# Kernel optimization log

Measured on AMD Instinct MI355X. Metric: run time of the kernel, lower is better.

The kernel has to match this reference:

```python
import jax, jax.numpy as jnp
import numpy as np

DEPTH = 6
N_LEAF = 2 ** DEPTH          # 64
GATE_COUNT = N_LEAF - 1      # 63
B = 1024
GATING_FEATURES = 512
IN_FEATURES = 512
OUT_FEATURES = 512


def setup_inputs() -> dict:
    key = jax.random.key(0)
    k1, k2, k3, k4 = jax.random.split(key, 4)
    x_gating = jax.random.normal(k1, (B, GATING_FEATURES), dtype=jnp.float32)
    x_leaf = jax.random.normal(k2, (B, IN_FEATURES), dtype=jnp.float32)
    # kaiming-normal-ish init scales
    gw = jax.random.normal(k3, (GATING_FEATURES, GATE_COUNT), dtype=jnp.float32) * (1.0 / np.sqrt(GATING_FEATURES))
    gb = jnp.zeros((GATE_COUNT,), dtype=jnp.float32)
    pw = jax.random.normal(k4, (OUT_FEATURES, IN_FEATURES, N_LEAF), dtype=jnp.float32) * (1.0 / np.sqrt(IN_FEATURES))
    pb = jnp.zeros((OUT_FEATURES, N_LEAF), dtype=jnp.float32)
    return {"x_gating": x_gating, "x_leaf": x_leaf, "gw": gw, "gb": gb, "pw": pw, "pb": pb}


def _leaf_probs(x_gating, gw, gb):
    # gatings: (B, gate_count), internal nodes in breadth-first order
    gatings = jax.nn.sigmoid(x_gating @ gw + gb)
    b = gatings.shape[0]
    dens = jnp.ones((b, 1), dtype=gatings.dtype)  # root density
    start = 0
    for d in range(DEPTH):
        n_par = 2 ** d
        g = gatings[:, start:start + n_par]          # (B, n_par)
        # left child (even it+1) gets g, right child gets 1-g, interleaved
        dens = jnp.stack([dens * g, dens * (1.0 - g)], axis=-1).reshape(b, 2 * n_par)
        start += n_par
    return dens  # (B, n_leaf) = leaf densities (last n_leaf node densities)


def reference(x_gating, x_leaf, gw, gb, pw, pb):
    leaf_probs = _leaf_probs(x_gating, gw, gb)              # (B, L)
    # gated projection applied to x_leaf, summed over leaves:
    # equals ((pw @ leaf_probs.T).permute(2,0,1) @ x_leaf[...,None])[...,0]
    result = jnp.einsum('oil,bl,bi->bo', pw, leaf_probs, x_leaf)
    result = result + leaf_probs @ pb.T                     # gated bias (B, O)
    return result
```

## Files before the change

kernel.cpp:

```cpp
#include <hip/hip_runtime.h>
#include <stdint.h>

#define B_SZ   1024
#define GF     512
#define GC     63
#define NLEAF  64
#define IN_F   512
#define OUT_F  512

typedef float f32x4 __attribute__((ext_vector_type(4)));
typedef __fp16 h16x2 __attribute__((ext_vector_type(2)));
typedef __fp16 h16x8 __attribute__((ext_vector_type(8)));
typedef _Float16 f16x2 __attribute__((ext_vector_type(2)));

union HF8 { f16x2 h2[4]; h16x8 v; uint4 u; };

__device__ inline f16x2 pkrtz(float a, float b) {
  union { h16x2 r; f16x2 f; } u;
  u.r = __builtin_amdgcn_cvt_pkrtz(a, b);
  return u.f;
}

__global__ __launch_bounds__(512, 2) void k_leafprobs(
    const float* __restrict__ xg, const float* __restrict__ gw,
    const float* __restrict__ gb, float* __restrict__ p_ws)
{
  __shared__ float xsr[GF];
  __shared__ float part[512];
  __shared__ float gates[GC + 1];
  const int b = blockIdx.x;
  const int t = threadIdx.x;

  xsr[t] = xg[(size_t)b * GF + t];
  __syncthreads();

  const int ks = t >> 6, g = t & 63;
  float acc = 0.f;
  if (g < GC) {
    const float* gp = gw + (size_t)(ks * 64) * GC + g;
    const float* xp = &xsr[ks * 64];
#pragma unroll 8
    for (int k = 0; k < 64; ++k) acc += xp[k] * gp[(size_t)k * GC];
  }
  part[t] = acc;
  __syncthreads();

  if (t < GC) {
    float s = gb[t];
#pragma unroll
    for (int r = 0; r < 8; ++r) s += part[r * 64 + t];
    gates[t] = 1.f / (1.f + expf(-s));
  }
  __syncthreads();

  if (t < NLEAF) {
    float v = 1.f;
    int idx = 0, start = 0;
#pragma unroll
    for (int d = 0; d < 6; ++d) {
      int bit = (t >> (5 - d)) & 1;
      float gg = gates[start + idx];
      v *= bit ? (1.f - gg) : gg;
      idx = 2 * idx + bit;
      start += (1 << d);
    }
    p_ws[(size_t)b * NLEAF + t] = v;
  }
}

#define SK 16
#define KI 32

template <bool ATOMIC>
__global__ __launch_bounds__(256, 2) void k_fused(
    const float* __restrict__ x_leaf,
    const float* __restrict__ p_ws,
    const float* __restrict__ pw,
    float* __restrict__ dst)
{
  __shared__ __align__(16) float         xs[KI][256];
  __shared__ __align__(16) unsigned char bs8[2 * 16384];

  const int tid  = threadIdx.x;
  const int lane = tid & 63;
  const int wid  = tid >> 6;
  const int quad = lane >> 4;
  const int l15  = lane & 15;
  const int l7   = l15 & 7;

  const int bid = blockIdx.x;
  const int nt  = bid & 7;
  const int mt  = (bid >> 3) & 3;
  const int kc  = bid >> 5;

  const int row_m0 = mt * 256;
  const int o0     = nt * 64;
  const int i0     = kc * KI;
  const int wm     = wid * 64;

  {
    const float* src = x_leaf + (size_t)(row_m0 + tid) * IN_F + i0;
#pragma unroll
    for (int q = 0; q < 8; ++q) {
      float4 v = *(const float4*)(src + q * 4);
      xs[q * 4 + 0][tid] = v.x;
      xs[q * 4 + 1][tid] = v.y;
      xs[q * 4 + 2][tid] = v.z;
      xs[q * 4 + 3][tid] = v.w;
    }
  }

  HF8 prh[4][2];
#pragma unroll
  for (int mi = 0; mi < 4; ++mi) {
    const int row = row_m0 + wm + mi * 16 + l15;
#pragma unroll
    for (int ks = 0; ks < 2; ++ks) {
      const f32x4* src = (const f32x4*)(p_ws + (size_t)row * NLEAF + ks * 32 + quad * 8);
      f32x4 lo = src[0], hi = src[1];
      prh[mi][ks].h2[0] = pkrtz(lo[0], lo[1]);
      prh[mi][ks].h2[1] = pkrtz(lo[2], lo[3]);
      prh[mi][ks].h2[2] = pkrtz(hi[0], hi[1]);
      prh[mi][ks].h2[3] = pkrtz(hi[2], hi[3]);
    }
  }

  const int br  = tid >> 2;
  const int seg = tid & 3;
  const float* bsrc0 = pw + ((size_t)(o0 + br) * IN_F + i0) * NLEAF + seg * 16;

  const int wsw   = (br & 7) << 4;
  const int woff0 = br * 128 + ((seg * 32) ^ wsw);
  const int woff1 = br * 128 + ((seg * 32 + 16) ^ wsw);
  int coff[2];
#pragma unroll
  for (int ks = 0; ks < 2; ++ks)
    coff[ks] = (ks * 64 + quad * 16) ^ (l7 << 4);
  const int rbase = l15 * 128;

  f32x4 acc[4][4];
#pragma unroll
  for (int mi = 0; mi < 4; ++mi)
#pragma unroll
    for (int ni = 0; ni < 4; ++ni)
      acc[mi][ni] = (f32x4)(0.f);

  f32x4 rb[4][4];

#define BLOAD(T, SLOT)                                                        \
  {                                                                           \
    const float* a_ = bsrc0 + (size_t)(T) * NLEAF;                            \
    asm volatile(                                                             \
        "global_load_dwordx4 %0, %4, off\n\t"                                 \
        "global_load_dwordx4 %1, %4, off offset:16\n\t"                       \
        "global_load_dwordx4 %2, %4, off offset:32\n\t"                       \
        "global_load_dwordx4 %3, %4, off offset:48"                           \
        : "=&v"(rb[SLOT][0]), "=&v"(rb[SLOT][1]),                             \
          "=&v"(rb[SLOT][2]), "=&v"(rb[SLOT][3])                              \
        : "v"(a_) : "memory");                                                \
  }

#define BWAIT_(SLOT, N)                                                       \
  asm volatile("s_waitcnt vmcnt(" #N ")"                                      \
               : "+v"(rb[SLOT][0]), "+v"(rb[SLOT][1]),                        \
                 "+v"(rb[SLOT][2]), "+v"(rb[SLOT][3])::"memory");             \
  __builtin_amdgcn_sched_barrier(0);
#define BWAIT(SLOT, N) BWAIT_(SLOT, N)

#define BSTAGE(SLOT, BUF, SUB)                                                \
  {                                                                           \
    HF8 c0_, c1_;                                                             \
    f32x4 a0_ = rb[SLOT][0], a1_ = rb[SLOT][1];                               \
    f32x4 a2_ = rb[SLOT][2], a3_ = rb[SLOT][3];                               \
    c0_.h2[0] = pkrtz(a0_[0], a0_[1]);                                        \
    c0_.h2[1] = pkrtz(a0_[2], a0_[3]);                                        \
    c0_.h2[2] = pkrtz(a1_[0], a1_[1]);                                        \
    c0_.h2[3] = pkrtz(a1_[2], a1_[3]);                                        \
    c1_.h2[0] = pkrtz(a2_[0], a2_[1]);                                        \
    c1_.h2[1] = pkrtz(a2_[2], a2_[3]);                                        \
    c1_.h2[2] = pkrtz(a3_[0], a3_[1]);                                        \
    c1_.h2[3] = pkrtz(a3_[2], a3_[3]);                                        \
    unsigned char* d_ = bs8 + (BUF) * 16384 + (SUB) * 8192;                   \
    *(uint4*)(d_ + woff0) = c0_.u;                                            \
    *(uint4*)(d_ + woff1) = c1_.u;                                            \
  }

#define BARRIER() asm volatile("s_waitcnt lgkmcnt(0)\n\ts_barrier" ::: "memory")

#define COMPUTE(IT, BUF, SUB)                                                 \
  {                                                                           \
    float xvf[4];                                                             \
    _Float16 xh[4];                                                           \
    _Pragma("unroll")                                                         \
    for (int mi = 0; mi < 4; ++mi) xvf[mi] = xs[(IT)][wm + mi * 16 + l15];    \
    _Pragma("unroll")                                                         \
    for (int mi = 0; mi < 4; ++mi) xh[mi] = (_Float16)xvf[mi];                \
    const unsigned char* bsr_ = bs8 + (BUF) * 16384 + (SUB) * 8192;           \
    __builtin_amdgcn_s_setprio(1);                                            \
    _Pragma("unroll")                                                         \
    for (int ks = 0; ks < 2; ++ks) {                                          \
      h16x8 af[4];                                                            \
      _Pragma("unroll")                                                       \
      for (int mi = 0; mi < 4; ++mi) {                                        \
        HF8 t_;                                                               \
        f16x2 xp_; xp_[0] = xh[mi]; xp_[1] = xh[mi];                          \
        _Pragma("unroll")                                                     \
        for (int j = 0; j < 4; ++j) t_.h2[j] = prh[mi][ks].h2[j] * xp_;       \
        af[mi] = t_.v;                                                        \
      }                                                                       \
      _Pragma("unroll")                                                       \
      for (int ni = 0; ni < 4; ++ni) {                                        \
        h16x8 bfr = *(const h16x8*)(bsr_ + ni * 2048 + rbase + coff[ks]);     \
        _Pragma("unroll")                                                     \
        for (int mi = 0; mi < 4; ++mi)                                        \
          acc[mi][ni] = __builtin_amdgcn_mfma_f32_16x16x32_f16(               \
              af[mi], bfr, acc[mi][ni], 0, 0, 0);                             \
      }                                                                       \
    }                                                                         \
    __builtin_amdgcn_s_setprio(0);                                            \
  }

#define PHASE(IT0, BUF, SA, SB, WA, WB, DLA, DLB)                             \
  {                                                                           \
    COMPUTE(IT0, BUF, 0)                                                      \
    BWAIT(SA, WA)                                                             \
    BSTAGE(SA, (BUF) ^ 1, 0)                                                  \
    if (DLA) { BLOAD((IT0) + 6, SA) }                                         \
    COMPUTE((IT0) + 1, BUF, 1)                                                \
    BWAIT(SB, WB)                                                             \
    BSTAGE(SB, (BUF) ^ 1, 1)                                                  \
    if (DLB) { BLOAD((IT0) + 7, SB) }                                         \
    BARRIER();                                                                \
  }

  BLOAD(0, 0)
  BLOAD(1, 1)
  BLOAD(2, 2)
  BLOAD(3, 3)
  BWAIT(0, 12)
  BSTAGE(0, 0, 0)
  BWAIT(1, 8)
  BSTAGE(1, 0, 1)
  BLOAD(4, 0)
  BLOAD(5, 1)
  BARRIER();

  for (int pp = 0; pp < 24; pp += 8) {
    PHASE(pp + 0, 0, 2, 3, 12, 12, 1, 1)
    PHASE(pp + 2, 1, 0, 1, 12, 12, 1, 1)
    PHASE(pp + 4, 0, 2, 3, 12, 12, 1, 1)
    PHASE(pp + 6, 1, 0, 1, 12, 12, 1, 1)
  }
  PHASE(24, 0, 2, 3, 12, 12, 1, 1)
  PHASE(26, 1, 0, 1, 12, 8, 0, 0)
  PHASE(28, 0, 2, 3, 4, 0, 0, 0)
  COMPUTE(30, 1, 0)
  COMPUTE(31, 1, 1)

#undef BLOAD
#undef BWAIT
#undef BWAIT_
#undef BSTAGE
#undef BARRIER
#undef COMPUTE
#undef PHASE

#pragma unroll
  for (int mi = 0; mi < 4; ++mi) {
#pragma unroll
    for (int ni = 0; ni < 4; ++ni) {
      int row = row_m0 + wm + mi * 16 + quad * 4;
      int col = o0 + ni * 16 + l15;
      if (ATOMIC) {
        float* o = dst + (size_t)row * OUT_F + col;
        atomicAdd(o,             acc[mi][ni][0]);
        atomicAdd(o + OUT_F,     acc[mi][ni][1]);
        atomicAdd(o + 2 * OUT_F, acc[mi][ni][2]);
        atomicAdd(o + 3 * OUT_F, acc[mi][ni][3]);
      } else {
        float* o = dst + ((size_t)kc << 19) + (size_t)row * OUT_F + col;
        o[0]         = acc[mi][ni][0];
        o[OUT_F]     = acc[mi][ni][1];
        o[2 * OUT_F] = acc[mi][ni][2];
        o[3 * OUT_F] = acc[mi][ni][3];
      }
    }
  }
}

__global__ __launch_bounds__(256, 4) void k_reduce(
    const float* __restrict__ parts, const float* __restrict__ p_ws,
    const float* __restrict__ pb, float* __restrict__ out, int nparts)
{
  __shared__ float ps_l[2 * NLEAF];
  const int t  = threadIdx.x;
  const int b0 = blockIdx.x * 2;

  if (t < 32)
    ((f32x4*)ps_l)[t] = ((const f32x4*)(p_ws + (size_t)b0 * NLEAF))[t];
  __syncthreads();

  const int row = b0 + (t >> 7);
  const int c0  = (t & 127) * 4;
  const f32x4* ps = (const f32x4*)&ps_l[(t >> 7) * NLEAF];

  f32x4 a;
#pragma unroll
  for (int jo = 0; jo < 4; ++jo) {
    const f32x4* pbo = (const f32x4*)(pb + (size_t)(c0 + jo) * NLEAF);
    f32x4 s = (f32x4)(0.f);
#pragma unroll
    for (int lv = 0; lv < 16; ++lv) s += pbo[lv] * ps[lv];
    a[jo] = s[0] + s[1] + s[2] + s[3];
  }

#pragma unroll 8
  for (int k = 0; k < nparts; ++k)
    a += *(const f32x4*)(parts + ((size_t)k << 19) + (size_t)row * OUT_F + c0);

  *(f32x4*)(out + (size_t)row * OUT_F + c0) = a;
}

extern "C" void kernel_launch(void* const* d_in, const int* in_sizes, int n_in,
                              void* d_out, int out_size, void* d_ws, size_t ws_size,
                              hipStream_t stream) {
  const float* xg = (const float*)d_in[0];
  const float* xl = (const float*)d_in[1];
  const float* gw = (const float*)d_in[2];
  const float* gb = (const float*)d_in[3];
  const float* pw = (const float*)d_in[4];
  const float* pb = (const float*)d_in[5];
  float* out = (float*)d_out;

  const size_t P_BYTES = (size_t)B_SZ * NLEAF * 4;
  const size_t SLICE   = (size_t)B_SZ * OUT_F * 4;

  float* p_ws  = (float*)d_ws;
  float* parts = (float*)((char*)d_ws + P_BYTES);

  k_leafprobs<<<dim3(B_SZ), dim3(512), 0, stream>>>(xg, gw, gb, p_ws);

  if (ws_size >= P_BYTES + SK * SLICE) {
    k_fused<false><<<dim3(512), dim3(256), 0, stream>>>(xl, p_ws, pw, parts);
    k_reduce<<<dim3(512), dim3(256), 0, stream>>>(parts, p_ws, pb, out, SK);
  } else {
    k_reduce<<<dim3(512), dim3(256), 0, stream>>>(parts, p_ws, pb, out, 0);
    k_fused<true><<<dim3(512), dim3(256), 0, stream>>>(xl, p_ws, pw, out);
  }
}
```

Baseline: 166.5 us.

## Software-pipeline A-fragment prep and fold gated bias into fused MFMA kernel

Splits the compute step into a PREP stage (scaling leaf probs by x into fp16 A fragments) and an MFMA stage. The next sub-iteration's fragments are prepared while the current MFMAs issue, and a sched_barrier is dropped so the compiler can interleave more freely. The gated bias (leaf_probs @ pb.T) moves into the split-K slice kc==0 as one extra MFMA pass using pb staged as fp16, which leaves k_reduce as a plain sum over slices. The cost is more live registers for the double A fragments, fp16 precision on the bias, and an extra barrier plus MFMA work on a subset of blocks.

New measurement: 146.4 us. 1.14x faster.

```diff
diff --git a/kernel.cpp b/kernel.cpp
--- a/kernel.cpp
+++ b/kernel.cpp
@@ -76,6 +76,7 @@
     const float* __restrict__ x_leaf,
     const float* __restrict__ p_ws,
     const float* __restrict__ pw,
+    const float* __restrict__ pb,
     float* __restrict__ dst)
 {
   __shared__ __align__(16) float         xs[KI][256];
@@ -146,6 +147,7 @@
       acc[mi][ni] = (f32x4)(0.f);
 
   f32x4 rb[4][4];
+  HF8 afA[2][4], afB[2][4];
 
 #define BLOAD(T, SLOT)                                                        \
   {                                                                           \
@@ -163,8 +165,7 @@
 #define BWAIT_(SLOT, N)                                                       \
   asm volatile("s_waitcnt vmcnt(" #N ")"                                      \
                : "+v"(rb[SLOT][0]), "+v"(rb[SLOT][1]),                        \
-                 "+v"(rb[SLOT][2]), "+v"(rb[SLOT][3])::"memory");             \
-  __builtin_amdgcn_sched_barrier(0);
+                 "+v"(rb[SLOT][2]), "+v"(rb[SLOT][3])::"memory");
 #define BWAIT(SLOT, N) BWAIT_(SLOT, N)
 
 #define BSTAGE(SLOT, BUF, SUB)                                                \
@@ -187,7 +188,7 @@
 
 #define BARRIER() asm volatile("s_waitcnt lgkmcnt(0)\n\ts_barrier" ::: "memory")
 
-#define COMPUTE(IT, BUF, SUB)                                                 \
+#define PREP(IT, AF)                                                          \
   {                                                                           \
     float xvf[4];                                                             \
     _Float16 xh[4];                                                           \
@@ -195,38 +196,44 @@
     for (int mi = 0; mi < 4; ++mi) xvf[mi] = xs[(IT)][wm + mi * 16 + l15];    \
     _Pragma("unroll")                                                         \
     for (int mi = 0; mi < 4; ++mi) xh[mi] = (_Float16)xvf[mi];                \
+    _Pragma("unroll")                                                         \
+    for (int ks = 0; ks < 2; ++ks) {                                          \
+      _Pragma("unroll")                                                       \
+      for (int mi = 0; mi < 4; ++mi) {                                        \
+        f16x2 xp_; xp_[0] = xh[mi]; xp_[1] = xh[mi];                          \
+        _Pragma("unroll")                                                     \
+        for (int j = 0; j < 4; ++j) AF[ks][mi].h2[j] = prh[mi][ks].h2[j] * xp_; \
+      }                                                                       \
+    }                                                                         \
+  }
+
+#define MFMAC(AF, BUF, SUB)                                                   \
+  {                                                                           \
     const unsigned char* bsr_ = bs8 + (BUF) * 16384 + (SUB) * 8192;           \
     __builtin_amdgcn_s_setprio(1);                                            \
     _Pragma("unroll")                                                         \
     for (int ks = 0; ks < 2; ++ks) {                                          \
-      h16x8 af[4];                                                            \
-      _Pragma("unroll")                                                       \
-      for (int mi = 0; mi < 4; ++mi) {                                        \
-        HF8 t_;                                                               \
-        f16x2 xp_; xp_[0] = xh[mi]; xp_[1] = xh[mi];                          \
-        _Pragma("unroll")                                                     \
-        for (int j = 0; j < 4; ++j) t_.h2[j] = prh[mi][ks].h2[j] * xp_;       \
-        af[mi] = t_.v;                                                        \
-      }                                                                       \
       _Pragma("unroll")                                                       \
       for (int ni = 0; ni < 4; ++ni) {                                        \
         h16x8 bfr = *(const h16x8*)(bsr_ + ni * 2048 + rbase + coff[ks]);     \
         _Pragma("unroll")                                                     \
         for (int mi = 0; mi < 4; ++mi)                                        \
           acc[mi][ni] = __builtin_amdgcn_mfma_f32_16x16x32_f16(               \
-              af[mi], bfr, acc[mi][ni], 0, 0, 0);                             \
+              AF[ks][mi].v, bfr, acc[mi][ni], 0, 0, 0);                       \
       }                                                                       \
     }                                                                         \
     __builtin_amdgcn_s_setprio(0);                                            \
   }
 
-#define PHASE(IT0, BUF, SA, SB, WA, WB, DLA, DLB)                             \
-  {                                                                           \
-    COMPUTE(IT0, BUF, 0)                                                      \
+#define PHASE(IT0, BUF, SA, SB, WA, WB, DLA, DLB, PN)                         \
+  {                                                                           \
+    PREP((IT0) + 1, afB)                                                      \
+    MFMAC(afA, BUF, 0)                                                        \
     BWAIT(SA, WA)                                                             \
     BSTAGE(SA, (BUF) ^ 1, 0)                                                  \
     if (DLA) { BLOAD((IT0) + 6, SA) }                                         \
-    COMPUTE((IT0) + 1, BUF, 1)                                                \
+    if (PN)  { PREP((IT0) + 2, afA) }                                         \
+    MFMAC(afB, BUF, 1)                                                        \
     BWAIT(SB, WB)                                                             \
     BSTAGE(SB, (BUF) ^ 1, 1)                                                  \
     if (DLB) { BLOAD((IT0) + 7, SB) }                                         \
@@ -244,26 +251,63 @@
   BLOAD(4, 0)
   BLOAD(5, 1)
   BARRIER();
+  PREP(0, afA)
 
   for (int pp = 0; pp < 24; pp += 8) {
-    PHASE(pp + 0, 0, 2, 3, 12, 12, 1, 1)
-    PHASE(pp + 2, 1, 0, 1, 12, 12, 1, 1)
-    PHASE(pp + 4, 0, 2, 3, 12, 12, 1, 1)
-    PHASE(pp + 6, 1, 0, 1, 12, 12, 1, 1)
-  }
-  PHASE(24, 0, 2, 3, 12, 12, 1, 1)
-  PHASE(26, 1, 0, 1, 12, 8, 0, 0)
-  PHASE(28, 0, 2, 3, 4, 0, 0, 0)
-  COMPUTE(30, 1, 0)
-  COMPUTE(31, 1, 1)
+    PHASE(pp + 0, 0, 2, 3, 12, 12, 1, 1, 1)
+    PHASE(pp + 2, 1, 0, 1, 12, 12, 1, 1, 1)
+    PHASE(pp + 4, 0, 2, 3, 12, 12, 1, 1, 1)
+    PHASE(pp + 6, 1, 0, 1, 12, 12, 1, 1, 1)
+  }
+  PHASE(24, 0, 2, 3, 12, 12, 1, 1, 1)
+  PHASE(26, 1, 0, 1, 12, 8, 0, 0, 1)
+  PHASE(28, 0, 2, 3, 4, 0, 0, 0, 1)
+  PREP(31, afB)
+  MFMAC(afA, 1, 0)
+  MFMAC(afB, 1, 1)
 
 #undef BLOAD
 #undef BWAIT
 #undef BWAIT_
 #undef BSTAGE
 #undef BARRIER
-#undef COMPUTE
+#undef PREP
+#undef MFMAC
 #undef PHASE
+
+  if (kc == 0) {
+    {
+      const float* pbs = pb + (size_t)(o0 + br) * NLEAF + seg * 16;
+      float4 a0_ = *(const float4*)(pbs);
+      float4 a1_ = *(const float4*)(pbs + 4);
+      float4 a2_ = *(const float4*)(pbs + 8);
+      float4 a3_ = *(const float4*)(pbs + 12);
+      HF8 c0_, c1_;
+      c0_.h2[0] = pkrtz(a0_.x, a0_.y);
+      c0_.h2[1] = pkrtz(a0_.z, a0_.w);
+      c0_.h2[2] = pkrtz(a1_.x, a1_.y);
+      c0_.h2[3] = pkrtz(a1_.z, a1_.w);
+      c1_.h2[0] = pkrtz(a2_.x, a2_.y);
+      c1_.h2[1] = pkrtz(a2_.z, a2_.w);
+      c1_.h2[2] = pkrtz(a3_.x, a3_.y);
+      c1_.h2[3] = pkrtz(a3_.z, a3_.w);
+      *(uint4*)(bs8 + woff0) = c0_.u;
+      *(uint4*)(bs8 + woff1) = c1_.u;
+    }
+    __syncthreads();
+    const unsigned char* bsr_ = bs8;
+#pragma unroll
+    for (int ks = 0; ks < 2; ++ks) {
+#pragma unroll
+      for (int ni = 0; ni < 4; ++ni) {
+        h16x8 bfr = *(const h16x8*)(bsr_ + ni * 2048 + rbase + coff[ks]);
+#pragma unroll
+        for (int mi = 0; mi < 4; ++mi)
+          acc[mi][ni] = __builtin_amdgcn_mfma_f32_16x16x32_f16(
+              prh[mi][ks].v, bfr, acc[mi][ni], 0, 0, 0);
+      }
+    }
+  }
 
 #pragma unroll
   for (int mi = 0; mi < 4; ++mi) {
@@ -288,37 +332,15 @@
   }
 }
 
-__global__ __launch_bounds__(256, 4) void k_reduce(
-    const float* __restrict__ parts, const float* __restrict__ p_ws,
-    const float* __restrict__ pb, float* __restrict__ out, int nparts)
+__global__ __launch_bounds__(256, 8) void k_reduce(
+    const float* __restrict__ parts, float* __restrict__ out, int nparts)
 {
-  __shared__ float ps_l[2 * NLEAF];
-  const int t  = threadIdx.x;
-  const int b0 = blockIdx.x * 2;
-
-  if (t < 32)
-    ((f32x4*)ps_l)[t] = ((const f32x4*)(p_ws + (size_t)b0 * NLEAF))[t];
-  __syncthreads();
-
-  const int row = b0 + (t >> 7);
-  const int c0  = (t & 127) * 4;
-  const f32x4* ps = (const f32x4*)&ps_l[(t >> 7) * NLEAF];
-
-  f32x4 a;
-#pragma unroll
-  for (int jo = 0; jo < 4; ++jo) {
-    const f32x4* pbo = (const f32x4*)(pb + (size_t)(c0 + jo) * NLEAF);
-    f32x4 s = (f32x4)(0.f);
-#pragma unroll
-    for (int lv = 0; lv < 16; ++lv) s += pbo[lv] * ps[lv];
-    a[jo] = s[0] + s[1] + s[2] + s[3];
-  }
-
+  const int idx = blockIdx.x * 256 + threadIdx.x;
+  f32x4 a = (f32x4)(0.f);
 #pragma unroll 8
   for (int k = 0; k < nparts; ++k)
-    a += *(const f32x4*)(parts + ((size_t)k << 19) + (size_t)row * OUT_F + c0);
-
-  *(f32x4*)(out + (size_t)row * OUT_F + c0) = a;
+    a += ((const f32x4*)(parts + ((size_t)k << 19)))[idx];
+  ((f32x4*)out)[idx] = a;
 }
 
 extern "C" void kernel_launch(void* const* d_in, const int* in_sizes, int n_in,
@@ -341,10 +363,10 @@
   k_leafprobs<<<dim3(B_SZ), dim3(512), 0, stream>>>(xg, gw, gb, p_ws);
 
   if (ws_size >= P_BYTES + SK * SLICE) {
-    k_fused<false><<<dim3(512), dim3(256), 0, stream>>>(xl, p_ws, pw, parts);
-    k_reduce<<<dim3(512), dim3(256), 0, stream>>>(parts, p_ws, pb, out, SK);
+    k_fused<false><<<dim3(512), dim3(256), 0, stream>>>(xl, p_ws, pw, pb, parts);
+    k_reduce<<<dim3(512), dim3(256), 0, stream>>>(parts, out, SK);
   } else {
-    k_reduce<<<dim3(512), dim3(256), 0, stream>>>(parts, p_ws, pb, out, 0);
-    k_fused<true><<<dim3(512), dim3(256), 0, stream>>>(xl, p_ws, pw, out);
-  }
-}
+    k_reduce<<<dim3(512), dim3(256), 0, stream>>>(parts, out, 0);
+    k_fused<true><<<dim3(512), dim3(256), 0, stream>>>(xl, p_ws, pw, pb, out);
+  }
+}
```
